# Kernel optimization log

Measured on AMD Instinct MI355X. Metric: run time of the kernel, lower is better.

## Reference

```python
import jax, jax.numpy as jnp
import numpy as np

N = 50000      # nodes
E = 800000     # directed edges (avg degree 16)
F_IN = 128     # input_size
HID = 128      # hidden_size
OUT = 64       # output_size (bottleneck)
EPS = 1e-5     # BatchNorm eps


def setup_inputs() -> dict:
    key = jax.random.key(0)
    ks = jax.random.split(key, 8)
    x = jax.random.normal(ks[0], (N, F_IN), dtype=jnp.float32)
    edge_index = jax.random.randint(ks[1], (2, E), 0, N, dtype=jnp.int64)
    dims = [(F_IN, HID), (HID, HID), (HID, OUT),   # encoder
            (OUT, HID), (HID, HID), (HID, F_IN)]   # decoder
    wkeys = jax.random.split(ks[2], 6)
    inp = {"x": x, "edge_index": edge_index}
    for j, (fi, fo) in enumerate(dims):
        inp[f"W{j}"] = jax.random.normal(wkeys[j], (fi, fo), dtype=jnp.float32) / np.sqrt(fi).astype(np.float32)
        inp[f"b{j}"] = jnp.zeros((fo,), dtype=jnp.float32)
        inp[f"g{j}"] = jnp.ones((fo,), dtype=jnp.float32)   # BN gamma
        inp[f"be{j}"] = jnp.zeros((fo,), dtype=jnp.float32)  # BN beta
    return inp


def _gcn(x, W, b, src, dst, edge_norm, inv_deg):
    # GCNConv: x' = D^-1/2 (A+I) D^-1/2 (x W) + b, sum-aggregation over edges
    h = x @ W                                   # [N, Fo]
    msg = h[src] * edge_norm[:, None]            # [E, Fo] gather + scale
    agg = jax.ops.segment_sum(msg, dst, num_segments=N)  # scatter-add
    agg = agg + h * inv_deg[:, None]             # self-loop term (norm = 1/deg)
    return agg + b


def _bn(x, g, be):
    # BatchNorm1d over nodes, training-mode batch statistics (biased var)
    m = jnp.mean(x, axis=0)
    v = jnp.mean((x - m) ** 2, axis=0)
    return (x - m) * jax.lax.rsqrt(v + EPS) * g + be


def _forward(x, edge_index, Ws, bs, gs, bes):
    src, dst = edge_index[0], edge_index[1]
    # degrees with self-loops (GCN adds self-loops, counts incoming edges)
    deg = jnp.zeros((N,), dtype=x.dtype).at[dst].add(1.0) + 1.0
    dinv_sqrt = jax.lax.rsqrt(deg)
    edge_norm = dinv_sqrt[src] * dinv_sqrt[dst]
    inv_deg = 1.0 / deg
    h = x
    for j in range(6):
        h = _gcn(h, Ws[j], bs[j], src, dst, edge_norm, inv_deg)
        h = _bn(h, gs[j], bes[j])
        if j not in (2, 5):  # ReLU after first two layers of each GNN, not after bn3
            h = jax.nn.relu(h)
    return h


def reference(x, edge_index,
              W0, b0, g0, be0, W1, b1, g1, be1, W2, b2, g2, be2,
              W3, b3, g3, be3, W4, b4, g4, be4, W5, b5, g5, be5):
    Ws = (W0, W1, W2, W3, W4, W5)
    bs = (b0, b1, b2, b3, b4, b5)
    gs = (g0, g1, g2, g3, g4, g5)
    bes = (be0, be1, be2, be3, be4, be5)
    return _forward(x, edge_index, Ws, bs, gs, bes)
```

## Files before the change

### kernel.cpp

```cpp
#include <hip/hip_runtime.h>
#include <hip/hip_bf16.h>

#define N_NODES 50000
#define N_EDGES 800000
constexpr float BN_EPS = 1e-5f;
constexpr int NCHUNK = (N_NODES + 1023) / 1024;

typedef unsigned short ushortT;
typedef float fx4 __attribute__((ext_vector_type(4)));

__device__ __forceinline__ unsigned short f2bf(float f) {
    __hip_bfloat16 h = __float2bfloat16(f);
    return __builtin_bit_cast(unsigned short, h);
}
__device__ __forceinline__ void cvt4(uint2 v, float* f) {
    f[0] = __uint_as_float(v.x << 16); f[1] = __uint_as_float(v.x & 0xffff0000u);
    f[2] = __uint_as_float(v.y << 16); f[3] = __uint_as_float(v.y & 0xffff0000u);
}


__global__ void count_deg(const int* __restrict__ dst, int* cnts) {
    int e = blockIdx.x * 256 + threadIdx.x;
    if (e < N_EDGES) atomicAdd(&cnts[dst[e]], 1);
}

__global__ void finalize_deg(const int* __restrict__ cnts, float* __restrict__ dinv,
                             float* __restrict__ invdeg) {
    int i = blockIdx.x * 256 + threadIdx.x;
    if (i < N_NODES) {
        float d = (float)cnts[i] + 1.0f;
        dinv[i] = rsqrtf(d);
        invdeg[i] = 1.0f / d;
    }
}

__global__ __launch_bounds__(256)
void scan_block_sums(const int* __restrict__ counts, int* __restrict__ totals) {
    __shared__ int red[4];
    int tid = threadIdx.x;
    int base = blockIdx.x * 1024 + tid * 4;
    int s = 0;
    #pragma unroll
    for (int j = 0; j < 4; ++j) { int i = base + j; if (i < N_NODES) s += counts[i]; }
    #pragma unroll
    for (int d = 1; d < 64; d <<= 1) s += __shfl_xor(s, d, 64);
    if ((tid & 63) == 0) red[tid >> 6] = s;
    __syncthreads();
    if (tid == 0) totals[blockIdx.x] = red[0] + red[1] + red[2] + red[3];
}

__global__ __launch_bounds__(256)
void scan_write(const int* __restrict__ counts, const int* __restrict__ totals,
                int* __restrict__ offs, int* __restrict__ cursor) {
    __shared__ int chunkbase;
    __shared__ int wsum[4];
    int tid = threadIdx.x, lane = tid & 63, wid = tid >> 6;
    if (tid == 0) { int a = 0; for (int i = 0; i < (int)blockIdx.x; ++i) a += totals[i]; chunkbase = a; }
    int base = blockIdx.x * 1024 + tid * 4;
    int v[4]; int s = 0;
    #pragma unroll
    for (int j = 0; j < 4; ++j) { int i = base + j; v[j] = (i < N_NODES) ? counts[i] : 0; s += v[j]; }
    int ts = s;
    #pragma unroll
    for (int d = 1; d < 64; d <<= 1) { int t = __shfl_up(ts, d, 64); if (lane >= d) ts += t; }
    if (lane == 63) wsum[wid] = ts;
    __syncthreads();
    int wbase = 0;
    #pragma unroll
    for (int w = 0; w < 4; ++w) if (w < wid) wbase += wsum[w];
    int excl = chunkbase + wbase + (ts - s);
    #pragma unroll
    for (int j = 0; j < 4; ++j) {
        int i = base + j;
        if (i < N_NODES) { offs[i] = excl; cursor[i] = excl; }
        excl += v[j];
    }
}

__global__ void fill_csr(const int* __restrict__ src, const int* __restrict__ dst,
                         const float* __restrict__ dinv, int* cursor,
                         uint2* __restrict__ edges) {
    int e = blockIdx.x * 256 + threadIdx.x;
    if (e < N_EDGES) {
        int s = src[e], d = dst[e];
        int pos = atomicAdd(&cursor[d], 1);
        edges[pos] = make_uint2((unsigned)s, __float_as_uint(dinv[s] * dinv[d]));
    }
}


template<int FI, int FO, bool BN, bool RELU>
__global__ __launch_bounds__(256)
void gemm_bn(const float* __restrict__ X, const float* __restrict__ W,
             ushortT* __restrict__ Hb, const float* __restrict__ stats_prev,
             const float* __restrict__ g_prev, const float* __restrict__ be_prev) {
    constexpr int CT = FO / 4;
    constexpr int RT = 256 / CT;
    constexpr int ROWS = RT * 4;
    __shared__ ushortT Ws[FI * FO];
    __shared__ float xs[ROWS * FI];
    __shared__ float sscale[FI], sshift[FI];
    if constexpr (BN) {
        if (threadIdx.x < FI) {
            constexpr float invN = 1.0f / (float)N_NODES;
            int k = threadIdx.x;
            float m = stats_prev[k] * invN;
            float var = stats_prev[FI + k] * invN - m * m;
            float is = rsqrtf(var + BN_EPS) * g_prev[k];
            sscale[k] = is;
            sshift[k] = be_prev[k] - m * is;
        }
    }
    for (int i = threadIdx.x * 8; i < FI * FO; i += 256 * 8) {
        float4 w0 = *(const float4*)&W[i];
        float4 w1 = *(const float4*)&W[i + 4];
        ushortT us[8] = { f2bf(w0.x), f2bf(w0.y), f2bf(w0.z), f2bf(w0.w),
                          f2bf(w1.x), f2bf(w1.y), f2bf(w1.z), f2bf(w1.w) };
        *(uint4*)&Ws[i] = *(uint4*)us;
    }
    const int ct = threadIdx.x % CT, rt = threadIdx.x / CT;
    const int col = ct * 4;
    ushortT* Hcol = Hb + (size_t)(col >> 5) * N_NODES * 32 + (col & 31);
    const int ntiles = (N_NODES + ROWS - 1) / ROWS;
    for (int tile = blockIdx.x; tile < ntiles; tile += gridDim.x) {
        const int base = tile * ROWS;
        __syncthreads();
        for (int t = threadIdx.x; t < ROWS * FI / 4; t += 256) {
            int r = t / (FI / 4), k4 = (t % (FI / 4)) * 4;
            int gr = base + r;
            float4 v = (gr < N_NODES) ? *(const float4*)&X[(size_t)gr * FI + k4]
                                      : make_float4(0.f, 0.f, 0.f, 0.f);
            if constexpr (BN) {
                float4 sc = *(const float4*)&sscale[k4];
                float4 sh = *(const float4*)&sshift[k4];
                v.x = fmaf(v.x, sc.x, sh.x); v.y = fmaf(v.y, sc.y, sh.y);
                v.z = fmaf(v.z, sc.z, sh.z); v.w = fmaf(v.w, sc.w, sh.w);
                if constexpr (RELU) {
                    v.x = fmaxf(v.x, 0.f); v.y = fmaxf(v.y, 0.f);
                    v.z = fmaxf(v.z, 0.f); v.w = fmaxf(v.w, 0.f);
                }
            }
            *(float4*)&xs[r * FI + k4] = v;
        }
        __syncthreads();
        float acc[4][4] = {};
        #pragma unroll 2
        for (int k4 = 0; k4 < FI; k4 += 4) {
            float4 xv[4], wv[4];
            #pragma unroll
            for (int ri = 0; ri < 4; ++ri)
                xv[ri] = *(const float4*)&xs[(rt * 4 + ri) * FI + k4];
            #pragma unroll
            for (int j = 0; j < 4; ++j) {
                ushort4 wu = *(const ushort4*)&Ws[(k4 + j) * FO + col];
                wv[j] = make_float4(__uint_as_float((unsigned)wu.x << 16),
                                    __uint_as_float((unsigned)wu.y << 16),
                                    __uint_as_float((unsigned)wu.z << 16),
                                    __uint_as_float((unsigned)wu.w << 16));
            }
            #pragma unroll
            for (int ri = 0; ri < 4; ++ri) {
                #pragma unroll
                for (int j = 0; j < 4; ++j) {
                    float xk = ((const float*)&xv[ri])[j];
                    acc[ri][0] = fmaf(xk, wv[j].x, acc[ri][0]);
                    acc[ri][1] = fmaf(xk, wv[j].y, acc[ri][1]);
                    acc[ri][2] = fmaf(xk, wv[j].z, acc[ri][2]);
                    acc[ri][3] = fmaf(xk, wv[j].w, acc[ri][3]);
                }
            }
        }
        #pragma unroll
        for (int ri = 0; ri < 4; ++ri) {
            int row = base + rt * 4 + ri;
            if (row < N_NODES) {
                ushortT us[4] = { f2bf(acc[ri][0]), f2bf(acc[ri][1]),
                                  f2bf(acc[ri][2]), f2bf(acc[ri][3]) };
                *(ushort4*)&Hcol[(size_t)row * 32] = *(ushort4*)us;
            }
        }
    }
}


template<int FO>
__global__ __launch_bounds__(256)
void aggregate_sliced(const ushortT* __restrict__ Hb, const int* __restrict__ offs,
                      const int* __restrict__ cnt, const uint2* __restrict__ edges,
                      const float* __restrict__ invdeg, const float* __restrict__ bias,
                      float* __restrict__ out, float* __restrict__ stats) {
    constexpr int NPASS = FO / 32;
    constexpr int BPX = 8 / NPASS;
    const int b = blockIdx.x;
    const int pass = (b & 7) / BPX;
    const int bi = (b >> 3) * BPX + (b & 7) % BPX;
    const int NBP = gridDim.x / NPASS;
    const int lt = threadIdx.x & 7;
    const int sub = threadIdx.x >> 3;
    const uint2* S2 = (const uint2*)(Hb + (size_t)pass * N_NODES * 32);
    const int f0 = pass * 32 + lt * 4;
    float bb[4] = { bias[f0], bias[f0 + 1], bias[f0 + 2], bias[f0 + 3] };
    float s[4] = {}, s2[4] = {};
    for (int r = bi * 32 + sub; r < N_NODES; r += NBP * 32) {
        float idg = invdeg[r];
        float a[4], f[4];
        cvt4(S2[(size_t)r * 8 + lt], f);
        #pragma unroll
        for (int j = 0; j < 4; ++j) a[j] = fmaf(f[j], idg, bb[j]);
        int e = offs[r], en = e + cnt[r];
        for (; e + 2 <= en; e += 2) {
            uint2 ed0 = edges[e], ed1 = edges[e + 1];
            uint2 v0 = S2[(size_t)ed0.x * 8 + lt];
            uint2 v1 = S2[(size_t)ed1.x * 8 + lt];
            float w0 = __uint_as_float(ed0.y), w1 = __uint_as_float(ed1.y);
            float g0[4], g1[4];
            cvt4(v0, g0); cvt4(v1, g1);
            #pragma unroll
            for (int j = 0; j < 4; ++j) a[j] = fmaf(g0[j], w0, a[j]);
            #pragma unroll
            for (int j = 0; j < 4; ++j) a[j] = fmaf(g1[j], w1, a[j]);
        }
        if (e < en) {
            uint2 ed = edges[e];
            float w = __uint_as_float(ed.y);
            float g[4];
            cvt4(S2[(size_t)ed.x * 8 + lt], g);
            #pragma unroll
            for (int j = 0; j < 4; ++j) a[j] = fmaf(g[j], w, a[j]);
        }
        fx4 o4 = { a[0], a[1], a[2], a[3] };
        __builtin_nontemporal_store(o4, (fx4*)&out[(size_t)r * FO + f0]);
        #pragma unroll
        for (int j = 0; j < 4; ++j) { s[j] += a[j]; s2[j] += a[j] * a[j]; }
    }
    __shared__ float ls[256][4], ls2[256][4];
    #pragma unroll
    for (int j = 0; j < 4; ++j) { ls[threadIdx.x][j] = s[j]; ls2[threadIdx.x][j] = s2[j]; }
    __syncthreads();
    if (sub == 0) {
        for (int t = 1; t < 32; ++t) {
            #pragma unroll
            for (int j = 0; j < 4; ++j) {
                s[j] += ls[t * 8 + lt][j];
                s2[j] += ls2[t * 8 + lt][j];
            }
        }
        #pragma unroll
        for (int j = 0; j < 4; ++j) {
            atomicAdd(&stats[f0 + j], s[j]);
            atomicAdd(&stats[FO + f0 + j], s2[j]);
        }
    }
}


template<int FO, bool RELU>
__global__ __launch_bounds__(256)
void bn_norm(const float* __restrict__ X, const float* __restrict__ stats,
             const float* __restrict__ g, const float* __restrict__ be,
             float* __restrict__ Y) {
    constexpr float invN = 1.0f / (float)N_NODES;
    const int total4 = N_NODES * FO / 4;
    for (int idx = blockIdx.x * 256 + threadIdx.x; idx < total4; idx += gridDim.x * 256) {
        int o4 = (idx * 4) & (FO - 1);
        float4 x = ((const float4*)X)[idx];
        float y[4];
        #pragma unroll
        for (int j = 0; j < 4; ++j) {
            int o = o4 + j;
            float m = stats[o] * invN;
            float v = stats[FO + o] * invN - m * m;
            float istd = rsqrtf(v + BN_EPS);
            float val = ((&x.x)[j] - m) * istd * g[o] + be[o];
            if (RELU) val = fmaxf(val, 0.f);
            y[j] = val;
        }
        ((float4*)Y)[idx] = make_float4(y[0], y[1], y[2], y[3]);
    }
}


extern "C" void kernel_launch(void* const* d_in, const int* in_sizes, int n_in,
                              void* d_out, int out_size, void* d_ws, size_t ws_size,
                              hipStream_t stream) {
    const float* x  = (const float*)d_in[0];
    const int* ei   = (const int*)d_in[1];
    const int* src  = ei;
    const int* dst  = ei + N_EDGES;

    size_t off = 0;
    auto alloc = [&](size_t bytes) -> void* {
        void* p = (char*)d_ws + off;
        off += (bytes + 255) & ~(size_t)255;
        return p;
    };
    int*     counts = (int*)    alloc((size_t)N_NODES * 4);
    int*     offs   = (int*)    alloc((size_t)N_NODES * 4);
    int*     cursor = (int*)    alloc((size_t)N_NODES * 4);
    int*     totals = (int*)    alloc((size_t)NCHUNK * 4);
    float*   dinv   = (float*)  alloc((size_t)N_NODES * 4);
    float*   invdeg = (float*)  alloc((size_t)N_NODES * 4);
    uint2*   edges  = (uint2*)  alloc((size_t)N_EDGES * 8);
    float*   stats  = (float*)  alloc(6 * 256 * 4);
    ushortT* Hb     = (ushortT*)alloc((size_t)N_NODES * 128 * 2);
    float*   A0     = (float*)  alloc((size_t)N_NODES * 128 * 4);
    float*   A1     = (float*)  alloc((size_t)N_NODES * 128 * 4);

    hipMemsetAsync(counts, 0, (size_t)N_NODES * 4, stream);
    hipMemsetAsync(stats, 0, 6 * 256 * 4, stream);

    count_deg<<<(N_EDGES + 255) / 256, 256, 0, stream>>>(dst, counts);
    finalize_deg<<<(N_NODES + 255) / 256, 256, 0, stream>>>(counts, dinv, invdeg);
    scan_block_sums<<<NCHUNK, 256, 0, stream>>>(counts, totals);
    scan_write<<<NCHUNK, 256, 0, stream>>>(counts, totals, offs, cursor);
    fill_csr<<<(N_EDGES + 255) / 256, 256, 0, stream>>>(src, dst, dinv, cursor, edges);

    const float* W[6]; const float* b[6]; const float* g[6]; const float* be[6];
    for (int j = 0; j < 6; ++j) {
        W[j]  = (const float*)d_in[2 + 4 * j];
        b[j]  = (const float*)d_in[3 + 4 * j];
        g[j]  = (const float*)d_in[4 + 4 * j];
        be[j] = (const float*)d_in[5 + 4 * j];
    }
    float* st[6];
    for (int j = 0; j < 6; ++j) st[j] = stats + j * 256;
    float* dout = (float*)d_out;

    gemm_bn<128, 128, false, false><<<768, 256, 0, stream>>>(x, W[0], Hb, nullptr, nullptr, nullptr);
    aggregate_sliced<128><<<2048, 256, 0, stream>>>(Hb, offs, counts, edges, invdeg, b[0], A0, st[0]);

    gemm_bn<128, 128, true, true><<<768, 256, 0, stream>>>(A0, W[1], Hb, st[0], g[0], be[0]);
    aggregate_sliced<128><<<2048, 256, 0, stream>>>(Hb, offs, counts, edges, invdeg, b[1], A1, st[1]);

    gemm_bn<128, 64, true, true><<<768, 256, 0, stream>>>(A1, W[2], Hb, st[1], g[1], be[1]);
    aggregate_sliced<64><<<2048, 256, 0, stream>>>(Hb, offs, counts, edges, invdeg, b[2], A0, st[2]);

    gemm_bn<64, 128, true, false><<<768, 256, 0, stream>>>(A0, W[3], Hb, st[2], g[2], be[2]);
    aggregate_sliced<128><<<2048, 256, 0, stream>>>(Hb, offs, counts, edges, invdeg, b[3], A1, st[3]);

    gemm_bn<128, 128, true, true><<<768, 256, 0, stream>>>(A1, W[4], Hb, st[3], g[3], be[3]);
    aggregate_sliced<128><<<2048, 256, 0, stream>>>(Hb, offs, counts, edges, invdeg, b[4], A0, st[4]);

    gemm_bn<128, 128, true, true><<<768, 256, 0, stream>>>(A0, W[5], Hb, st[4], g[4], be[4]);
    aggregate_sliced<128><<<2048, 256, 0, stream>>>(Hb, offs, counts, edges, invdeg, b[5], dout, st[5]);
    bn_norm<128, false><<<2048, 256, 0, stream>>>(dout, st[5], g[5], be[5], dout);
}
```

Measured before the change: 937.8 us.

## Pack CSR edges to 32-bit with fp16 weights and fold self-loops into CSR

Each edge record shrinks from 8 bytes to 4: a 16-bit source index plus a half-precision norm weight. The self-loop becomes an extra CSR entry per node, and row bounds come from offs[r+1], so the aggregation no longer loads counts or invdeg. Rows are also split into contiguous ranges per block group, which should improve locality. The intent is to cut edge-stream bandwidth and per-row loads. The risks are fp16 weight rounding and a 16-bit index field that cannot represent node IDs of 65536 or more, which holds for N=50000 only.

```diff
diff --git a/kernel.cpp b/kernel.cpp
--- a/kernel.cpp
+++ b/kernel.cpp
@@ -1,5 +1,6 @@
 #include <hip/hip_runtime.h>
 #include <hip/hip_bf16.h>
+#include <hip/hip_fp16.h>
 
 #define N_NODES 50000
 #define N_EDGES 800000
@@ -17,6 +18,9 @@
     f[0] = __uint_as_float(v.x << 16); f[1] = __uint_as_float(v.x & 0xffff0000u);
     f[2] = __uint_as_float(v.y << 16); f[3] = __uint_as_float(v.y & 0xffff0000u);
 }
+__device__ __forceinline__ float dec_w(unsigned rec) {
+    return __half2float(__builtin_bit_cast(__half, (unsigned short)(rec >> 16)));
+}
 
 
 __global__ void count_deg(const int* __restrict__ dst, int* cnts) {
@@ -24,14 +28,9 @@
     if (e < N_EDGES) atomicAdd(&cnts[dst[e]], 1);
 }
 
-__global__ void finalize_deg(const int* __restrict__ cnts, float* __restrict__ dinv,
-                             float* __restrict__ invdeg) {
+__global__ void finalize_deg(const int* __restrict__ cnts, float* __restrict__ dinv) {
     int i = blockIdx.x * 256 + threadIdx.x;
-    if (i < N_NODES) {
-        float d = (float)cnts[i] + 1.0f;
-        dinv[i] = rsqrtf(d);
-        invdeg[i] = 1.0f / d;
-    }
+    if (i < N_NODES) dinv[i] = rsqrtf((float)cnts[i] + 1.0f);
 }
 
 __global__ __launch_bounds__(256)
@@ -41,7 +40,7 @@
     int base = blockIdx.x * 1024 + tid * 4;
     int s = 0;
     #pragma unroll
-    for (int j = 0; j < 4; ++j) { int i = base + j; if (i < N_NODES) s += counts[i]; }
+    for (int j = 0; j < 4; ++j) { int i = base + j; if (i < N_NODES) s += counts[i] + 1; }
     #pragma unroll
     for (int d = 1; d < 64; d <<= 1) s += __shfl_xor(s, d, 64);
     if ((tid & 63) == 0) red[tid >> 6] = s;
@@ -59,7 +58,7 @@
     int base = blockIdx.x * 1024 + tid * 4;
     int v[4]; int s = 0;
     #pragma unroll
-    for (int j = 0; j < 4; ++j) { int i = base + j; v[j] = (i < N_NODES) ? counts[i] : 0; s += v[j]; }
+    for (int j = 0; j < 4; ++j) { int i = base + j; v[j] = (i < N_NODES) ? counts[i] + 1 : 0; s += v[j]; }
     int ts = s;
     #pragma unroll
     for (int d = 1; d < 64; d <<= 1) { int t = __shfl_up(ts, d, 64); if (lane >= d) ts += t; }
@@ -74,17 +73,29 @@
         int i = base + j;
         if (i < N_NODES) { offs[i] = excl; cursor[i] = excl; }
         excl += v[j];
+        if (i == N_NODES - 1) offs[N_NODES] = excl;
     }
 }
 
 __global__ void fill_csr(const int* __restrict__ src, const int* __restrict__ dst,
                          const float* __restrict__ dinv, int* cursor,
-                         uint2* __restrict__ edges) {
+                         unsigned* __restrict__ edges) {
     int e = blockIdx.x * 256 + threadIdx.x;
     if (e < N_EDGES) {
         int s = src[e], d = dst[e];
         int pos = atomicAdd(&cursor[d], 1);
-        edges[pos] = make_uint2((unsigned)s, __float_as_uint(dinv[s] * dinv[d]));
+        unsigned short hb = __builtin_bit_cast(unsigned short, __float2half(dinv[s] * dinv[d]));
+        edges[pos] = (unsigned)s | ((unsigned)hb << 16);
+    }
+}
+
+__global__ void fill_self(const int* __restrict__ counts, const int* __restrict__ offs,
+                          unsigned* __restrict__ edges) {
+    int i = blockIdx.x * 256 + threadIdx.x;
+    if (i < N_NODES) {
+        float w = 1.0f / ((float)counts[i] + 1.0f);
+        unsigned short hb = __builtin_bit_cast(unsigned short, __float2half(w));
+        edges[offs[i] + counts[i]] = (unsigned)i | ((unsigned)hb << 16);
     }
 }
 
@@ -186,33 +197,33 @@
 template<int FO>
 __global__ __launch_bounds__(256)
 void aggregate_sliced(const ushortT* __restrict__ Hb, const int* __restrict__ offs,
-                      const int* __restrict__ cnt, const uint2* __restrict__ edges,
-                      const float* __restrict__ invdeg, const float* __restrict__ bias,
+                      const unsigned* __restrict__ edges, const float* __restrict__ bias,
                       float* __restrict__ out, float* __restrict__ stats) {
     constexpr int NPASS = FO / 32;
-    constexpr int BPX = 8 / NPASS;
+    constexpr int XPP = 8 / NPASS;
+    constexpr int RPX = N_NODES / XPP;
     const int b = blockIdx.x;
-    const int pass = (b & 7) / BPX;
-    const int bi = (b >> 3) * BPX + (b & 7) % BPX;
-    const int NBP = gridDim.x / NPASS;
+    const int b7 = b & 7;
+    const int pass = b7 / XPP;
+    const int rx = b7 % XPP;
+    const int o = b >> 3;
+    const int NB = gridDim.x >> 3;
+    const int r_lo = rx * RPX;
+    const int r_hi = r_lo + RPX;
     const int lt = threadIdx.x & 7;
     const int sub = threadIdx.x >> 3;
     const uint2* S2 = (const uint2*)(Hb + (size_t)pass * N_NODES * 32);
     const int f0 = pass * 32 + lt * 4;
-    float bb[4] = { bias[f0], bias[f0 + 1], bias[f0 + 2], bias[f0 + 3] };
+    const float4 b4 = *(const float4*)&bias[f0];
     float s[4] = {}, s2[4] = {};
-    for (int r = bi * 32 + sub; r < N_NODES; r += NBP * 32) {
-        float idg = invdeg[r];
-        float a[4], f[4];
-        cvt4(S2[(size_t)r * 8 + lt], f);
-        #pragma unroll
-        for (int j = 0; j < 4; ++j) a[j] = fmaf(f[j], idg, bb[j]);
-        int e = offs[r], en = e + cnt[r];
+    for (int r = r_lo + o * 32 + sub; r < r_hi; r += NB * 32) {
+        float a[4] = { b4.x, b4.y, b4.z, b4.w };
+        int e = offs[r], en = offs[r + 1];
         for (; e + 2 <= en; e += 2) {
-            uint2 ed0 = edges[e], ed1 = edges[e + 1];
-            uint2 v0 = S2[(size_t)ed0.x * 8 + lt];
-            uint2 v1 = S2[(size_t)ed1.x * 8 + lt];
-            float w0 = __uint_as_float(ed0.y), w1 = __uint_as_float(ed1.y);
+            uint2 ee = *(const uint2*)&edges[e];
+            uint2 v0 = S2[(size_t)(ee.x & 0xffff) * 8 + lt];
+            uint2 v1 = S2[(size_t)(ee.y & 0xffff) * 8 + lt];
+            float w0 = dec_w(ee.x), w1 = dec_w(ee.y);
             float g0[4], g1[4];
             cvt4(v0, g0); cvt4(v1, g1);
             #pragma unroll
@@ -221,10 +232,10 @@
             for (int j = 0; j < 4; ++j) a[j] = fmaf(g1[j], w1, a[j]);
         }
         if (e < en) {
-            uint2 ed = edges[e];
-            float w = __uint_as_float(ed.y);
+            unsigned ee = edges[e];
+            float w = dec_w(ee);
             float g[4];
-            cvt4(S2[(size_t)ed.x * 8 + lt], g);
+            cvt4(S2[(size_t)(ee & 0xffff) * 8 + lt], g);
             #pragma unroll
             for (int j = 0; j < 4; ++j) a[j] = fmaf(g[j], w, a[j]);
         }
@@ -294,26 +305,26 @@
         off += (bytes + 255) & ~(size_t)255;
         return p;
     };
-    int*     counts = (int*)    alloc((size_t)N_NODES * 4);
-    int*     offs   = (int*)    alloc((size_t)N_NODES * 4);
-    int*     cursor = (int*)    alloc((size_t)N_NODES * 4);
-    int*     totals = (int*)    alloc((size_t)NCHUNK * 4);
-    float*   dinv   = (float*)  alloc((size_t)N_NODES * 4);
-    float*   invdeg = (float*)  alloc((size_t)N_NODES * 4);
-    uint2*   edges  = (uint2*)  alloc((size_t)N_EDGES * 8);
-    float*   stats  = (float*)  alloc(6 * 256 * 4);
-    ushortT* Hb     = (ushortT*)alloc((size_t)N_NODES * 128 * 2);
-    float*   A0     = (float*)  alloc((size_t)N_NODES * 128 * 4);
-    float*   A1     = (float*)  alloc((size_t)N_NODES * 128 * 4);
-
-    hipMemsetAsync(counts, 0, (size_t)N_NODES * 4, stream);
-    hipMemsetAsync(stats, 0, 6 * 256 * 4, stream);
+    int*      counts = (int*)     alloc((size_t)N_NODES * 4);
+    int*      offs   = (int*)     alloc((size_t)(N_NODES + 1) * 4);
+    int*      cursor = (int*)     alloc((size_t)N_NODES * 4);
+    int*      totals = (int*)     alloc((size_t)NCHUNK * 4);
+    float*    dinv   = (float*)   alloc((size_t)N_NODES * 4);
+    unsigned* edges  = (unsigned*)alloc((size_t)(N_EDGES + N_NODES) * 4);
+    float*    stats  = (float*)   alloc(6 * 256 * 4);
+    ushortT*  Hb     = (ushortT*) alloc((size_t)N_NODES * 128 * 2);
+    float*    A0     = (float*)   alloc((size_t)N_NODES * 128 * 4);
+    float*    A1     = (float*)   alloc((size_t)N_NODES * 128 * 4);
+
+    (void)hipMemsetAsync(counts, 0, (size_t)N_NODES * 4, stream);
+    (void)hipMemsetAsync(stats, 0, 6 * 256 * 4, stream);
 
     count_deg<<<(N_EDGES + 255) / 256, 256, 0, stream>>>(dst, counts);
-    finalize_deg<<<(N_NODES + 255) / 256, 256, 0, stream>>>(counts, dinv, invdeg);
+    finalize_deg<<<(N_NODES + 255) / 256, 256, 0, stream>>>(counts, dinv);
     scan_block_sums<<<NCHUNK, 256, 0, stream>>>(counts, totals);
     scan_write<<<NCHUNK, 256, 0, stream>>>(counts, totals, offs, cursor);
     fill_csr<<<(N_EDGES + 255) / 256, 256, 0, stream>>>(src, dst, dinv, cursor, edges);
+    fill_self<<<(N_NODES + 255) / 256, 256, 0, stream>>>(counts, offs, edges);
 
     const float* W[6]; const float* b[6]; const float* g[6]; const float* be[6];
     for (int j = 0; j < 6; ++j) {
@@ -327,21 +338,21 @@
     float* dout = (float*)d_out;
 
     gemm_bn<128, 128, false, false><<<768, 256, 0, stream>>>(x, W[0], Hb, nullptr, nullptr, nullptr);
-    aggregate_sliced<128><<<2048, 256, 0, stream>>>(Hb, offs, counts, edges, invdeg, b[0], A0, st[0]);
+    aggregate_sliced<128><<<2048, 256, 0, stream>>>(Hb, offs, edges, b[0], A0, st[0]);
 
     gemm_bn<128, 128, true, true><<<768, 256, 0, stream>>>(A0, W[1], Hb, st[0], g[0], be[0]);
-    aggregate_sliced<128><<<2048, 256, 0, stream>>>(Hb, offs, counts, edges, invdeg, b[1], A1, st[1]);
+    aggregate_sliced<128><<<2048, 256, 0, stream>>>(Hb, offs, edges, b[1], A1, st[1]);
 
     gemm_bn<128, 64, true, true><<<768, 256, 0, stream>>>(A1, W[2], Hb, st[1], g[1], be[1]);
-    aggregate_sliced<64><<<2048, 256, 0, stream>>>(Hb, offs, counts, edges, invdeg, b[2], A0, st[2]);
+    aggregate_sliced<64><<<2048, 256, 0, stream>>>(Hb, offs, edges, b[2], A0, st[2]);
 
     gemm_bn<64, 128, true, false><<<768, 256, 0, stream>>>(A0, W[3], Hb, st[2], g[2], be[2]);
-    aggregate_sliced<128><<<2048, 256, 0, stream>>>(Hb, offs, counts, edges, invdeg, b[3], A1, st[3]);
+    aggregate_sliced<128><<<2048, 256, 0, stream>>>(Hb, offs, edges, b[3], A1, st[3]);
 
     gemm_bn<128, 128, true, true><<<768, 256, 0, stream>>>(A1, W[4], Hb, st[3], g[3], be[3]);
-    aggregate_sliced<128><<<2048, 256, 0, stream>>>(Hb, offs, counts, edges, invdeg, b[4], A0, st[4]);
+    aggregate_sliced<128><<<2048, 256, 0, stream>>>(Hb, offs, edges, b[4], A0, st[4]);
 
     gemm_bn<128, 128, true, true><<<768, 256, 0, stream>>>(A0, W[5], Hb, st[4], g[4], be[4]);
-    aggregate_sliced<128><<<2048, 256, 0, stream>>>(Hb, offs, counts, edges, invdeg, b[5], dout, st[5]);
+    aggregate_sliced<128><<<2048, 256, 0, stream>>>(Hb, offs, edges, b[5], dout, st[5]);
     bn_norm<128, false><<<2048, 256, 0, stream>>>(dout, st[5], g[5], be[5], dout);
 }
```

New measurement: 929.3 us. No clear change (-0.9%).
